# Kernel optimization log

Measured on AMD Instinct MI355X. Metric: run time of the kernel, lower is better.

## Reference

```python
import jax, jax.numpy as jnp
import numpy as np

N = 100000      # nodes
E = 1600000     # edges (before self loops)
F_IN = 128      # input features
HID = 64        # hidden_layer (heads=1)
G = 128         # number of graphs
NUM_CLASSES = 10


def _gat_layer(x, src, dst, W, a_src, a_dst, b):
    # x: [N, Fin] -> h: [N, HID]; single head, PyG GATConv defaults
    h = x @ W
    alpha_src = h @ a_src            # [N]
    alpha_dst = h @ a_dst            # [N]
    e = jax.nn.leaky_relu(alpha_src[src] + alpha_dst[dst], 0.2)   # [E+N]
    # segment softmax over incoming edges of each destination node
    m = jax.ops.segment_max(e, dst, num_segments=N)
    ex = jnp.exp(e - m[dst])
    denom = jax.ops.segment_sum(ex, dst, num_segments=N)
    alpha = ex / denom[dst]
    out = jax.ops.segment_sum(h[src] * alpha[:, None], dst, num_segments=N)
    return out + b


def setup_inputs() -> dict:
    key = jax.random.key(0)
    ks = jax.random.split(key, 16)
    x = jax.random.normal(ks[0], (N, F_IN), dtype=jnp.float32)
    edge_index = jax.random.randint(ks[1], (2, E), 0, N, dtype=jnp.int64)
    edge_weight = jax.random.uniform(ks[2], (E,), dtype=jnp.float32)
    batch = jnp.sort(jax.random.randint(ks[3], (N,), 0, G, dtype=jnp.int64))
    s = 0.1
    params = {
        'W1': jax.random.normal(ks[4], (F_IN, HID), jnp.float32) * s,
        'a_src1': jax.random.normal(ks[5], (HID,), jnp.float32) * s,
        'a_dst1': jax.random.normal(ks[6], (HID,), jnp.float32) * s,
        'b1': jnp.zeros((HID,), jnp.float32),
        'W2': jax.random.normal(ks[7], (HID, HID), jnp.float32) * s,
        'a_src2': jax.random.normal(ks[8], (HID,), jnp.float32) * s,
        'a_dst2': jax.random.normal(ks[9], (HID,), jnp.float32) * s,
        'b2': jnp.zeros((HID,), jnp.float32),
        'lin_w': jax.random.normal(ks[10], (HID, HID // 2), jnp.float32) * s,
        'lin_b': jnp.zeros((HID // 2,), jnp.float32),
        'cls_w': jax.random.normal(ks[11], (HID // 2, NUM_CLASSES), jnp.float32) * s,
        'cls_b': jnp.zeros((NUM_CLASSES,), jnp.float32),
    }
    return {'x': x, 'edge_index': edge_index, 'edge_weight': edge_weight, 'batch': batch, **params}


def reference(x, edge_index, edge_weight, batch,
              W1, a_src1, a_dst1, b1,
              W2, a_src2, a_dst2, b2,
              lin_w, lin_b, cls_w, cls_b):
    # PyG GATConv add_self_loops=True
    loops = jnp.arange(N, dtype=edge_index.dtype)
    src = jnp.concatenate([edge_index[0], loops])
    dst = jnp.concatenate([edge_index[1], loops])
    # edge_weight unused: GATConv built without edge_dim (lin_edge is None)
    h = _gat_layer(x, src, dst, W1, a_src1, a_dst1, b1)
    h = jax.nn.relu(h)
    h = _gat_layer(h, src, dst, W2, a_src2, a_dst2, b2)
    # global_mean_pool over graphs
    counts = jax.ops.segment_sum(jnp.ones((N,), h.dtype), batch, num_segments=G)
    pooled = jax.ops.segment_sum(h, batch, num_segments=G) / jnp.maximum(counts, 1.0)[:, None]
    z = jax.nn.relu(pooled @ lin_w + lin_b)       # dropout p=0 -> identity
    logits = z @ cls_w + cls_b
    return jax.nn.log_softmax(logits, axis=1)     # SSL=False -> deg_pred=0 omitted
```

## Files before the change

### kernel.cpp

```cpp
#include <hip/hip_runtime.h>
#include <hip/hip_bf16.h>

#define NN 100000
#define NE 1600000
#define NT (NE + NN)
#define FIN 128
#define HID 64
#define NG 128
#define NC 10
#define BSHIFT 8
#define NBUCK ((NN + 255) >> 8)
#define A2_EPB 4096
#define PCH 8

typedef __hip_bfloat16 bf16;

__device__ __forceinline__ float ldx(const void* p, size_t i, int f32flag) {
    return f32flag ? ((const float*)p)[i]
                   : __bfloat162float(((const bf16*)p)[i]);
}
__device__ __forceinline__ float b2f(unsigned short u) {
    return __uint_as_float((unsigned)u << 16);
}

__global__ void probe_kernel(const unsigned int* __restrict__ xw,
                             const int* __restrict__ ei,
                             int* __restrict__ flags) {
    if (threadIdx.x != 0 || blockIdx.x != 0) return;
    int f32 = 0;
    for (int i = 0; i < 64; i++) {
        unsigned int u = xw[i];
        float vl = __uint_as_float((u & 0xffffu) << 16);
        float vh = __uint_as_float(u & 0xffff0000u);
        if (!(fabsf(vl) < 1e10f)) f32 = 1;
        if (!(fabsf(vh) < 1e10f)) f32 = 1;
    }
    int i64 = 1;
    for (int i = 0; i < 64; i++)
        if (ei[2 * i + 1] != 0) i64 = 0;
    flags[0] = f32;
    flags[1] = i64;
}

__global__ __launch_bounds__(256) void cparams_kernel(
        const void* p0, const void* p1, const void* p2, const void* p3,
        const void* p4, const void* p5, const void* p6, const void* p7,
        const void* p8, const void* p9, const void* p10, const void* p11,
        const int* __restrict__ flags, float* __restrict__ Pf) {
    const void* ps[12] = {p0,p1,p2,p3,p4,p5,p6,p7,p8,p9,p10,p11};
    const int   sz[12] = {8192,64,64,64,4096,64,64,64,2048,32,320,10};
    const int f = flags[0];
    int off = 0;
    for (int t = 0; t < 12; t++) {
        for (int i = threadIdx.x; i < sz[t]; i += 256)
            Pf[off + i] = ldx(ps[t], i, f);
        off += sz[t];
    }
}

template <int K>
__global__ __launch_bounds__(256) void gemm_kernel(const void* __restrict__ X,
                                                   const float* __restrict__ Wf,
                                                   const float* __restrict__ va,
                                                   const float* __restrict__ vb,
                                                   unsigned char* __restrict__ H8,
                                                   float* __restrict__ AS,
                                                   float* __restrict__ AD,
                                                   const int* __restrict__ flags,
                                                   int force_f32) {
    constexpr int KC = 32;
    constexpr int XLD = KC + 4;
    __shared__ float Wl[KC * HID];
    __shared__ float Xl[64 * XLD];
    const int t = threadIdx.x;
    const int f = force_f32 ? 1 : flags[0];
    const int brow = blockIdx.x * 64;
    const int rt = (t >> 4) * 4;
    const int ct = (t & 15) * 4;
    float acc[4][4] = {};
    for (int kc = 0; kc < K; kc += KC) {
        for (int i = t; i < KC * HID / 4; i += 256)
            ((float4*)Wl)[i] = ((const float4*)(Wf + kc * HID))[i];
        for (int i = t; i < 64 * KC / 4; i += 256) {
            int rr = i >> 3, col = (i & 7) * 4;
            int grow = brow + rr; if (grow >= NN) grow = NN - 1;
            size_t gbase = (size_t)grow * K + kc + col;
            float4 o;
            if (f) {
                o = *(const float4*)((const float*)X + gbase);
            } else {
                ushort4 v = *(const ushort4*)((const bf16*)X + gbase);
                o.x = b2f(v.x); o.y = b2f(v.y); o.z = b2f(v.z); o.w = b2f(v.w);
            }
            *(float4*)&Xl[rr * XLD + col] = o;
        }
        __syncthreads();
        const float* xp = &Xl[rt * XLD];
        const float* wp = &Wl[ct];
#pragma unroll 2
        for (int k = 0; k < KC; k += 4) {
            float4 w0 = *(const float4*)(wp + (k + 0) * HID);
            float4 w1 = *(const float4*)(wp + (k + 1) * HID);
            float4 w2 = *(const float4*)(wp + (k + 2) * HID);
            float4 w3 = *(const float4*)(wp + (k + 3) * HID);
#pragma unroll
            for (int i = 0; i < 4; i++) {
                float4 xv = *(const float4*)(xp + i * XLD + k);
                acc[i][0] += xv.x * w0.x + xv.y * w1.x + xv.z * w2.x + xv.w * w3.x;
                acc[i][1] += xv.x * w0.y + xv.y * w1.y + xv.z * w2.y + xv.w * w3.y;
                acc[i][2] += xv.x * w0.z + xv.y * w1.z + xv.z * w2.z + xv.w * w3.z;
                acc[i][3] += xv.x * w0.w + xv.y * w1.w + xv.z * w2.w + xv.w * w3.w;
            }
        }
        __syncthreads();
    }
    float va4[4], vb4[4];
#pragma unroll
    for (int j = 0; j < 4; j++) { va4[j] = va[ct + j]; vb4[j] = vb[ct + j]; }
#pragma unroll
    for (int i = 0; i < 4; i++) {
        int row = brow + rt + i;
        unsigned pk = 0;
#pragma unroll
        for (int j = 0; j < 4; j++) {
            int q = (int)rintf(fminf(fmaxf(acc[i][j] * 16.f, -128.f), 127.f)) + 128;
            pk |= ((unsigned)q & 0xffu) << (8 * j);
        }
        if (row < NN)
            *(unsigned*)&H8[(size_t)row * HID + ct] = pk;
        float s1 = acc[i][0] * va4[0] + acc[i][1] * va4[1] + acc[i][2] * va4[2] + acc[i][3] * va4[3];
        float s2 = acc[i][0] * vb4[0] + acc[i][1] * vb4[1] + acc[i][2] * vb4[2] + acc[i][3] * vb4[3];
#pragma unroll
        for (int off = 8; off; off >>= 1) {
            s1 += __shfl_xor(s1, off);
            s2 += __shfl_xor(s2, off);
        }
        if ((t & 15) == 0 && row < NN) { AS[row] = s1; AD[row] = s2; }
    }
}

__global__ __launch_bounds__(256) void bhistA_kernel(const int* __restrict__ ei,
                                                     const int* __restrict__ flags,
                                                     int* __restrict__ gcnt) {
    __shared__ int lc[NBUCK];
    for (int i = threadIdx.x; i < NBUCK; i += 256) lc[i] = 0;
    __syncthreads();
    const int i64 = flags[1];
    const int base = blockIdx.x * 8192;
    for (int i = threadIdx.x; i < 8192; i += 256) {
        int e = base + i;
        if (e >= NT) break;
        int d;
        if (e < NE) { long idx = (long)NE + e; d = i64 ? ei[2 * idx] : ei[idx]; }
        else d = e - NE;
        if ((unsigned)d >= NN) d = 0;
        atomicAdd(&lc[d >> BSHIFT], 1);
    }
    __syncthreads();
    for (int i = threadIdx.x; i < NBUCK; i += 256)
        if (lc[i]) atomicAdd(&gcnt[i], lc[i]);
}

__global__ __launch_bounds__(64) void bscan_kernel(const int* __restrict__ gcnt,
                                                   int* __restrict__ gbase,
                                                   int* __restrict__ gcursor) {
    const int lane = threadIdx.x;
    int carry = 0;
    for (int base = 0; base < NBUCK; base += 64) {
        int idx = base + lane;
        int v = (idx < NBUCK) ? gcnt[idx] : 0;
        int x = v;
#pragma unroll
        for (int off = 1; off < 64; off <<= 1) {
            int y = __shfl_up(x, off);
            if (lane >= off) x += y;
        }
        int excl = carry + x - v;
        if (idx < NBUCK) { gbase[idx] = excl; gcursor[idx] = excl; }
        carry += __shfl(x, 63);
    }
    if (lane == 0) gbase[NBUCK] = carry;
}

__global__ __launch_bounds__(256) void bscat_kernel(const int* __restrict__ ei,
                                                    const int* __restrict__ flags,
                                                    int* __restrict__ gcursor,
                                                    int2* __restrict__ bucketA) {
    __shared__ int lc[NBUCK];
    __shared__ int lpos[NBUCK];
    __shared__ int lcur[NBUCK];
    for (int i = threadIdx.x; i < NBUCK; i += 256) { lc[i] = 0; lcur[i] = 0; }
    __syncthreads();
    const int i64 = flags[1];
    const int base = blockIdx.x * A2_EPB;
    int sarr[16], darr[16];
#pragma unroll
    for (int i = 0; i < 16; i++) {
        int e = base + i * 256 + threadIdx.x;
        int s = -1, d = 0;
        if (e < NT) {
            if (e < NE) {
                s = i64 ? ei[2 * (long)e] : ei[e];
                long idx = (long)NE + e;
                d = i64 ? ei[2 * idx] : ei[idx];
            } else s = d = e - NE;
            if ((unsigned)d >= NN) d = 0;
            if ((unsigned)s >= NN) s = 0;
            atomicAdd(&lc[d >> BSHIFT], 1);
        }
        sarr[i] = s; darr[i] = d;
    }
    __syncthreads();
    for (int i = threadIdx.x; i < NBUCK; i += 256)
        lpos[i] = lc[i] ? atomicAdd(&gcursor[i], lc[i]) : 0;
    __syncthreads();
#pragma unroll
    for (int i = 0; i < 16; i++) {
        if (sarr[i] >= 0) {
            int b = darr[i] >> BSHIFT;
            int off = atomicAdd(&lcur[b], 1);
            bucketA[lpos[b] + off] = make_int2(sarr[i], darr[i]);
        }
    }
}

__global__ __launch_bounds__(256) void csr_kernel(const int2* __restrict__ bucketA,
                                                  const int* __restrict__ gbase,
                                                  int* __restrict__ rowptr,
                                                  int* __restrict__ slot) {
    const int b = blockIdx.x;
    const int nbase = b << BSHIFT;
    const int nb = min(256, NN - nbase);
    const int ebeg = gbase[b], eend = gbase[b + 1];
    __shared__ int cnt[256];
    __shared__ int excl[257];
    __shared__ int cur[256];
    const int t = threadIdx.x;
    cnt[t] = 0; cur[t] = 0;
    __syncthreads();
    for (int i = ebeg + t; i < eend; i += 256)
        atomicAdd(&cnt[bucketA[i].y - nbase], 1);
    __syncthreads();
    if (t < 64) {
        int carry = 0;
        for (int s0 = 0; s0 < 256; s0 += 64) {
            int v = cnt[s0 + t];
            int x = v;
#pragma unroll
            for (int off = 1; off < 64; off <<= 1) {
                int y = __shfl_up(x, off);
                if (t >= off) x += y;
            }
            excl[s0 + t] = carry + x - v;
            carry += __shfl(x, 63);
        }
        if (t == 0) excl[256] = carry;
    }
    __syncthreads();
    if (t < nb) rowptr[nbase + t] = ebeg + excl[t];
    if (b == NBUCK - 1 && t == 0) rowptr[NN] = ebeg + excl[nb];
    for (int i = ebeg + t; i < eend; i += 256) {
        int2 ed = bucketA[i];
        int dl = ed.y - nbase;
        int pos = atomicAdd(&cur[dl], 1);
        slot[ebeg + excl[dl] + pos] = ed.x;
    }
}

__global__ __launch_bounds__(256) void edge_kernel(const unsigned char* __restrict__ H8,
                                                   const float* __restrict__ AS,
                                                   const float* __restrict__ AD,
                                                   const int* __restrict__ rowptr,
                                                   const int* __restrict__ slot,
                                                   const float* __restrict__ bias,
                                                   float* __restrict__ OUT,
                                                   int relu_flag) {
    int wid = (blockIdx.x * 256 + threadIdx.x) >> 6;
    int lane = threadIdx.x & 63;
    if (wid >= NN) return;
    const int beg = rowptr[wid], end = rowptr[wid + 1];
    const float ad = AD[wid];
    const int sub = lane >> 4;
    const int fq  = (lane & 15) * 4;
    float a0 = 0.f, a1 = 0.f, a2 = 0.f, a3 = 0.f, dsum = 0.f;
    for (int cbeg = beg; cbeg < end; cbeg += 64) {
        int j = cbeg + lane;
        float ex = 0.f; int s = 0;
        if (j < end) {
            s = slot[j];
            float e = AS[s] + ad;
            e = e > 0.f ? e : 0.2f * e;
            ex = __expf(e);
            dsum += ex;
        }
        int cn = min(64, end - cbeg);
        for (int u = 0; u < cn; u += 8) {
            int   s0 = __shfl(s,  u + sub);
            float e0 = __shfl(ex, u + sub);
            int   s1 = __shfl(s,  u + 4 + sub);
            float e1 = __shfl(ex, u + 4 + sub);
            unsigned w0 = *(const unsigned*)(H8 + (size_t)s0 * HID + fq);
            unsigned w1 = *(const unsigned*)(H8 + (size_t)s1 * HID + fq);
            a0 += e0 * (float)( w0        & 0xffu);
            a1 += e0 * (float)((w0 >>  8) & 0xffu);
            a2 += e0 * (float)((w0 >> 16) & 0xffu);
            a3 += e0 * (float)( w0 >> 24        );
            a0 += e1 * (float)( w1        & 0xffu);
            a1 += e1 * (float)((w1 >>  8) & 0xffu);
            a2 += e1 * (float)((w1 >> 16) & 0xffu);
            a3 += e1 * (float)( w1 >> 24        );
        }
    }
    a0 += __shfl_xor(a0, 16); a0 += __shfl_xor(a0, 32);
    a1 += __shfl_xor(a1, 16); a1 += __shfl_xor(a1, 32);
    a2 += __shfl_xor(a2, 16); a2 += __shfl_xor(a2, 32);
    a3 += __shfl_xor(a3, 16); a3 += __shfl_xor(a3, 32);
#pragma unroll
    for (int off = 32; off; off >>= 1) dsum += __shfl_xor(dsum, off);
    if (lane < 16) {
        float inv = 0.0625f / dsum;
        float4 o;
        o.x = a0 * inv - 8.f + bias[fq + 0];
        o.y = a1 * inv - 8.f + bias[fq + 1];
        o.z = a2 * inv - 8.f + bias[fq + 2];
        o.w = a3 * inv - 8.f + bias[fq + 3];
        if (relu_flag) {
            o.x = fmaxf(o.x, 0.f); o.y = fmaxf(o.y, 0.f);
            o.z = fmaxf(o.z, 0.f); o.w = fmaxf(o.w, 0.f);
        }
        *(float4*)&OUT[(size_t)wid * HID + fq] = o;
    }
}

__global__ __launch_bounds__(256) void pool2a_kernel(const float* __restrict__ O,
                                                     const int* __restrict__ bat,
                                                     const int* __restrict__ flags,
                                                     float* __restrict__ part) {
    const int g = blockIdx.x / PCH;
    const int c = blockIdx.x % PCH;
    const int t = threadIdx.x;
    __shared__ int bnds[2];
    if (t < 2) {
        const int i64 = flags[1];
        int target = g + t;
        int lo = 0, hi = NN;
        while (lo < hi) {
            int mid = (lo + hi) >> 1;
            int v = i64 ? bat[2 * (long)mid] : bat[mid];
            if (v < target) lo = mid + 1; else hi = mid;
        }
        bnds[t] = lo;
    }
    __syncthreads();
    const int gbeg = bnds[0], gend = bnds[1];
    const int len = gend - gbeg;
    const int beg = gbeg + (int)((long)len * c / PCH);
    const int end = gbeg + (int)((long)len * (c + 1) / PCH);
    const int lane = t & 63;
    const int wv = t >> 6;
    float acc = 0.f;
    for (int i = beg + wv; i < end; i += 4)
        acc += O[(size_t)i * HID + lane];
    __shared__ float red[4][64];
    red[wv][lane] = acc;
    __syncthreads();
    if (wv == 0)
        part[(size_t)(g * PCH + c) * HID + lane] =
            red[0][lane] + red[1][lane] + red[2][lane] + red[3][lane];
}

__global__ __launch_bounds__(64) void pool2b_kernel(const float* __restrict__ part,
                                                    const int* __restrict__ bat,
                                                    const int* __restrict__ flags,
                                                    float* __restrict__ pooled) {
    const int g = blockIdx.x;
    const int t = threadIdx.x;
    __shared__ int bnds[2];
    if (t < 2) {
        const int i64 = flags[1];
        int target = g + t;
        int lo = 0, hi = NN;
        while (lo < hi) {
            int mid = (lo + hi) >> 1;
            int v = i64 ? bat[2 * (long)mid] : bat[mid];
            if (v < target) lo = mid + 1; else hi = mid;
        }
        bnds[t] = lo;
    }
    __syncthreads();
    float s = 0.f;
#pragma unroll
    for (int c = 0; c < PCH; c++)
        s += part[(size_t)(g * PCH + c) * HID + t];
    float cntg = (float)(bnds[1] - bnds[0]);
    pooled[g * HID + t] = s / fmaxf(cntg, 1.f);
}

__global__ __launch_bounds__(64) void head_kernel(const float* __restrict__ pooled,
                                                  const float* __restrict__ lw, const float* __restrict__ lb,
                                                  const float* __restrict__ cw, const float* __restrict__ cb,
                                                  float* __restrict__ out) {
    const int g = blockIdx.x;
    const int t = threadIdx.x;
    __shared__ float p[HID];
    __shared__ float z[32];
    __shared__ float lg[NC];
    p[t] = pooled[g * HID + t];
    __syncthreads();
    if (t < 32) {
        float acc = lb[t];
#pragma unroll
        for (int k = 0; k < HID; k++) acc += p[k] * lw[k * 32 + t];
        z[t] = fmaxf(acc, 0.f);
    }
    __syncthreads();
    if (t < NC) {
        float acc = cb[t];
#pragma unroll
        for (int j = 0; j < 32; j++) acc += z[j] * cw[j * NC + t];
        lg[t] = acc;
    }
    __syncthreads();
    if (t < NC) {
        float mx = -1e30f;
#pragma unroll
        for (int c = 0; c < NC; c++) mx = fmaxf(mx, lg[c]);
        float s = 0.f;
#pragma unroll
        for (int c = 0; c < NC; c++) s += __expf(lg[c] - mx);
        out[g * NC + t] = lg[t] - mx - __logf(s);
    }
}

extern "C" void kernel_launch(void* const* d_in, const int* in_sizes, int n_in,
                              void* d_out, int out_size, void* d_ws, size_t ws_size,
                              hipStream_t stream) {
    const void* x   = d_in[0];
    const int*  ei  = (const int*)d_in[1];
    const int*  bat = (const int*)d_in[3];

    char* w = (char*)d_ws;
    int2* bucketA = (int2*)w;  w += sizeof(int2) * NT;
    unsigned char* H8 = (unsigned char*)w; w += sizeof(char) * NN * HID;
    float* O      = (float*)w; w += sizeof(float) * NN * HID;
    float* AS     = (float*)w; w += sizeof(float) * NN;
    float* AD     = (float*)w; w += sizeof(float) * NN;
    int* rowptr   = (int*)w;   w += sizeof(int) * (NN + 1);
    int* slot     = (int*)w;   w += sizeof(int) * NT;
    float* part   = (float*)w; w += sizeof(float) * NG * PCH * HID;
    float* pooled = (float*)w; w += sizeof(float) * NG * HID;
    int* gcnt     = (int*)w;   w += sizeof(int) * NBUCK;
    int* gbase    = (int*)w;   w += sizeof(int) * (NBUCK + 1);
    int* gcursor  = (int*)w;   w += sizeof(int) * NBUCK;
    int* flags    = (int*)w;   w += sizeof(int) * 2;
    float* Pf     = (float*)w; w += sizeof(float) * 16384;

    float* W1f = Pf;             float* as1 = Pf + 8192;
    float* ad1 = Pf + 8256;      float* b1  = Pf + 8320;
    float* W2f = Pf + 8384;      float* as2 = Pf + 12480;
    float* ad2 = Pf + 12544;     float* b2  = Pf + 12608;
    float* lw  = Pf + 12672;     float* lb  = Pf + 14720;
    float* cw  = Pf + 14752;     float* cb  = Pf + 15072;

    hipMemsetAsync(gcnt, 0, sizeof(int) * NBUCK, stream);

    probe_kernel<<<1, 64, 0, stream>>>((const unsigned int*)x, ei, flags);
    cparams_kernel<<<1, 256, 0, stream>>>(d_in[4], d_in[5], d_in[6], d_in[7],
                                          d_in[8], d_in[9], d_in[10], d_in[11],
                                          d_in[12], d_in[13], d_in[14], d_in[15],
                                          flags, Pf);
    bhistA_kernel<<<(NT + 8191) / 8192, 256, 0, stream>>>(ei, flags, gcnt);
    bscan_kernel<<<1, 64, 0, stream>>>(gcnt, gbase, gcursor);
    bscat_kernel<<<(NT + A2_EPB - 1) / A2_EPB, 256, 0, stream>>>(ei, flags, gcursor, bucketA);
    csr_kernel<<<NBUCK, 256, 0, stream>>>(bucketA, gbase, rowptr, slot);
    gemm_kernel<FIN><<<(NN + 63) / 64, 256, 0, stream>>>(x, W1f, as1, ad1, H8, AS, AD, flags, 0);
    edge_kernel<<<NN / 4, 256, 0, stream>>>(H8, AS, AD, rowptr, slot, b1, O, 1);
    gemm_kernel<HID><<<(NN + 63) / 64, 256, 0, stream>>>(O, W2f, as2, ad2, H8, AS, AD, flags, 1);
    edge_kernel<<<NN / 4, 256, 0, stream>>>(H8, AS, AD, rowptr, slot, b2, O, 0);
    pool2a_kernel<<<NG * PCH, 256, 0, stream>>>(O, bat, flags, part);
    pool2b_kernel<<<NG, 64, 0, stream>>>(part, bat, flags, pooled);
    head_kernel<<<NG, 64, 0, stream>>>(pooled, lw, lb, cw, cb, (float*)d_out);
}
```

Baseline: 265.6 us.

## Merge setup kernels, pack edge buckets into int, store hidden as bf16

Three separate ideas are applied. The probe, param conversion and gcnt memset are merged into one setup kernel, and pool2b is merged with the head into a tail kernel, which cuts launch count. Bucketed edges are packed into a single int holding the 17-bit source and 8-bit local destination instead of an int2, halving scatter and CSR traffic. The layer outputs are now stored as bf16 instead of fp32, halving reads and writes for gemm2 and pooling at the cost of extra rounding error in hidden activations.

```diff
diff --git a/kernel.cpp b/kernel.cpp
--- a/kernel.cpp
+++ b/kernel.cpp
@@ -22,34 +22,37 @@
 __device__ __forceinline__ float b2f(unsigned short u) {
     return __uint_as_float((unsigned)u << 16);
 }
-
-__global__ void probe_kernel(const unsigned int* __restrict__ xw,
-                             const int* __restrict__ ei,
-                             int* __restrict__ flags) {
-    if (threadIdx.x != 0 || blockIdx.x != 0) return;
-    int f32 = 0;
-    for (int i = 0; i < 64; i++) {
-        unsigned int u = xw[i];
-        float vl = __uint_as_float((u & 0xffffu) << 16);
-        float vh = __uint_as_float(u & 0xffff0000u);
-        if (!(fabsf(vl) < 1e10f)) f32 = 1;
-        if (!(fabsf(vh) < 1e10f)) f32 = 1;
-    }
-    int i64 = 1;
-    for (int i = 0; i < 64; i++)
-        if (ei[2 * i + 1] != 0) i64 = 0;
-    flags[0] = f32;
-    flags[1] = i64;
-}
-
-__global__ __launch_bounds__(256) void cparams_kernel(
+__device__ __forceinline__ unsigned short f2b(float v) {
+    return (unsigned short)(__float_as_uint(v) >> 16);
+}
+
+__global__ __launch_bounds__(256) void setup_kernel(
+        const unsigned int* __restrict__ xw, const int* __restrict__ ei,
         const void* p0, const void* p1, const void* p2, const void* p3,
         const void* p4, const void* p5, const void* p6, const void* p7,
         const void* p8, const void* p9, const void* p10, const void* p11,
-        const int* __restrict__ flags, float* __restrict__ Pf) {
+        int* __restrict__ flags, int* __restrict__ gcnt, float* __restrict__ Pf) {
+    __shared__ int sf[2];
+    if (threadIdx.x == 0) {
+        int f32 = 0;
+        for (int i = 0; i < 64; i++) {
+            unsigned int u = xw[i];
+            float vl = __uint_as_float((u & 0xffffu) << 16);
+            float vh = __uint_as_float(u & 0xffff0000u);
+            if (!(fabsf(vl) < 1e10f)) f32 = 1;
+            if (!(fabsf(vh) < 1e10f)) f32 = 1;
+        }
+        int i64 = 1;
+        for (int i = 0; i < 64; i++)
+            if (ei[2 * i + 1] != 0) i64 = 0;
+        sf[0] = f32; sf[1] = i64;
+        flags[0] = f32; flags[1] = i64;
+    }
+    for (int i = threadIdx.x; i < NBUCK; i += 256) gcnt[i] = 0;
+    __syncthreads();
+    const int f = sf[0];
     const void* ps[12] = {p0,p1,p2,p3,p4,p5,p6,p7,p8,p9,p10,p11};
     const int   sz[12] = {8192,64,64,64,4096,64,64,64,2048,32,320,10};
-    const int f = flags[0];
     int off = 0;
     for (int t = 0; t < 12; t++) {
         for (int i = threadIdx.x; i < sz[t]; i += 256)
@@ -67,13 +70,13 @@
                                                    float* __restrict__ AS,
                                                    float* __restrict__ AD,
                                                    const int* __restrict__ flags,
-                                                   int force_f32) {
+                                                   int dtype_mode) {
     constexpr int KC = 32;
     constexpr int XLD = KC + 4;
     __shared__ float Wl[KC * HID];
     __shared__ float Xl[64 * XLD];
     const int t = threadIdx.x;
-    const int f = force_f32 ? 1 : flags[0];
+    const int f = (dtype_mode < 0) ? flags[0] : dtype_mode;
     const int brow = blockIdx.x * 64;
     const int rt = (t >> 4) * 4;
     const int ct = (t & 15) * 4;
@@ -185,7 +188,7 @@
 __global__ __launch_bounds__(256) void bscat_kernel(const int* __restrict__ ei,
                                                     const int* __restrict__ flags,
                                                     int* __restrict__ gcursor,
-                                                    int2* __restrict__ bucketA) {
+                                                    int* __restrict__ bucketA) {
     __shared__ int lc[NBUCK];
     __shared__ int lpos[NBUCK];
     __shared__ int lcur[NBUCK];
@@ -219,12 +222,12 @@
         if (sarr[i] >= 0) {
             int b = darr[i] >> BSHIFT;
             int off = atomicAdd(&lcur[b], 1);
-            bucketA[lpos[b] + off] = make_int2(sarr[i], darr[i]);
-        }
-    }
-}
-
-__global__ __launch_bounds__(256) void csr_kernel(const int2* __restrict__ bucketA,
+            bucketA[lpos[b] + off] = ((darr[i] & 0xff) << 17) | sarr[i];
+        }
+    }
+}
+
+__global__ __launch_bounds__(256) void csr_kernel(const int* __restrict__ bucketA,
                                                   const int* __restrict__ gbase,
                                                   int* __restrict__ rowptr,
                                                   int* __restrict__ slot) {
@@ -239,7 +242,7 @@
     cnt[t] = 0; cur[t] = 0;
     __syncthreads();
     for (int i = ebeg + t; i < eend; i += 256)
-        atomicAdd(&cnt[bucketA[i].y - nbase], 1);
+        atomicAdd(&cnt[bucketA[i] >> 17], 1);
     __syncthreads();
     if (t < 64) {
         int carry = 0;
@@ -260,10 +263,10 @@
     if (t < nb) rowptr[nbase + t] = ebeg + excl[t];
     if (b == NBUCK - 1 && t == 0) rowptr[NN] = ebeg + excl[nb];
     for (int i = ebeg + t; i < eend; i += 256) {
-        int2 ed = bucketA[i];
-        int dl = ed.y - nbase;
+        int v = bucketA[i];
+        int dl = v >> 17;
         int pos = atomicAdd(&cur[dl], 1);
-        slot[ebeg + excl[dl] + pos] = ed.x;
+        slot[ebeg + excl[dl] + pos] = v & 0x1ffff;
     }
 }
 
@@ -273,7 +276,7 @@
                                                    const int* __restrict__ rowptr,
                                                    const int* __restrict__ slot,
                                                    const float* __restrict__ bias,
-                                                   float* __restrict__ OUT,
+                                                   bf16* __restrict__ OUT,
                                                    int relu_flag) {
     int wid = (blockIdx.x * 256 + threadIdx.x) >> 6;
     int lane = threadIdx.x & 63;
@@ -319,20 +322,21 @@
     for (int off = 32; off; off >>= 1) dsum += __shfl_xor(dsum, off);
     if (lane < 16) {
         float inv = 0.0625f / dsum;
-        float4 o;
-        o.x = a0 * inv - 8.f + bias[fq + 0];
-        o.y = a1 * inv - 8.f + bias[fq + 1];
-        o.z = a2 * inv - 8.f + bias[fq + 2];
-        o.w = a3 * inv - 8.f + bias[fq + 3];
+        float ox = a0 * inv - 8.f + bias[fq + 0];
+        float oy = a1 * inv - 8.f + bias[fq + 1];
+        float oz = a2 * inv - 8.f + bias[fq + 2];
+        float ow = a3 * inv - 8.f + bias[fq + 3];
         if (relu_flag) {
-            o.x = fmaxf(o.x, 0.f); o.y = fmaxf(o.y, 0.f);
-            o.z = fmaxf(o.z, 0.f); o.w = fmaxf(o.w, 0.f);
-        }
-        *(float4*)&OUT[(size_t)wid * HID + fq] = o;
-    }
-}
-
-__global__ __launch_bounds__(256) void pool2a_kernel(const float* __restrict__ O,
+            ox = fmaxf(ox, 0.f); oy = fmaxf(oy, 0.f);
+            oz = fmaxf(oz, 0.f); ow = fmaxf(ow, 0.f);
+        }
+        ushort4 pk;
+        pk.x = f2b(ox); pk.y = f2b(oy); pk.z = f2b(oz); pk.w = f2b(ow);
+        *(ushort4*)&OUT[(size_t)wid * HID + fq] = pk;
+    }
+}
+
+__global__ __launch_bounds__(256) void pool2a_kernel(const bf16* __restrict__ O,
                                                      const int* __restrict__ bat,
                                                      const int* __restrict__ flags,
                                                      float* __restrict__ part) {
@@ -360,7 +364,7 @@
     const int wv = t >> 6;
     float acc = 0.f;
     for (int i = beg + wv; i < end; i += 4)
-        acc += O[(size_t)i * HID + lane];
+        acc += __bfloat162float(O[(size_t)i * HID + lane]);
     __shared__ float red[4][64];
     red[wv][lane] = acc;
     __syncthreads();
@@ -369,13 +373,18 @@
             red[0][lane] + red[1][lane] + red[2][lane] + red[3][lane];
 }
 
-__global__ __launch_bounds__(64) void pool2b_kernel(const float* __restrict__ part,
-                                                    const int* __restrict__ bat,
-                                                    const int* __restrict__ flags,
-                                                    float* __restrict__ pooled) {
+__global__ __launch_bounds__(64) void tail_kernel(const float* __restrict__ part,
+                                                  const int* __restrict__ bat,
+                                                  const int* __restrict__ flags,
+                                                  const float* __restrict__ lw, const float* __restrict__ lb,
+                                                  const float* __restrict__ cw, const float* __restrict__ cb,
+                                                  float* __restrict__ out) {
     const int g = blockIdx.x;
     const int t = threadIdx.x;
     __shared__ int bnds[2];
+    __shared__ float p[HID];
+    __shared__ float z[32];
+    __shared__ float lg[NC];
     if (t < 2) {
         const int i64 = flags[1];
         int target = g + t;
@@ -388,24 +397,12 @@
         bnds[t] = lo;
     }
     __syncthreads();
-    float s = 0.f;
+    float s0 = 0.f;
 #pragma unroll
     for (int c = 0; c < PCH; c++)
-        s += part[(size_t)(g * PCH + c) * HID + t];
+        s0 += part[(size_t)(g * PCH + c) * HID + t];
     float cntg = (float)(bnds[1] - bnds[0]);
-    pooled[g * HID + t] = s / fmaxf(cntg, 1.f);
-}
-
-__global__ __launch_bounds__(64) void head_kernel(const float* __restrict__ pooled,
-                                                  const float* __restrict__ lw, const float* __restrict__ lb,
-                                                  const float* __restrict__ cw, const float* __restrict__ cb,
-                                                  float* __restrict__ out) {
-    const int g = blockIdx.x;
-    const int t = threadIdx.x;
-    __shared__ float p[HID];
-    __shared__ float z[32];
-    __shared__ float lg[NC];
-    p[t] = pooled[g * HID + t];
+    p[t] = s0 / fmaxf(cntg, 1.f);
     __syncthreads();
     if (t < 32) {
         float acc = lb[t];
@@ -440,15 +437,14 @@
     const int*  bat = (const int*)d_in[3];
 
     char* w = (char*)d_ws;
-    int2* bucketA = (int2*)w;  w += sizeof(int2) * NT;
+    int* bucketA  = (int*)w;   w += sizeof(int) * NT;
     unsigned char* H8 = (unsigned char*)w; w += sizeof(char) * NN * HID;
-    float* O      = (float*)w; w += sizeof(float) * NN * HID;
+    bf16* Obf     = (bf16*)w;  w += sizeof(bf16) * NN * HID;
     float* AS     = (float*)w; w += sizeof(float) * NN;
     float* AD     = (float*)w; w += sizeof(float) * NN;
     int* rowptr   = (int*)w;   w += sizeof(int) * (NN + 1);
     int* slot     = (int*)w;   w += sizeof(int) * NT;
     float* part   = (float*)w; w += sizeof(float) * NG * PCH * HID;
-    float* pooled = (float*)w; w += sizeof(float) * NG * HID;
     int* gcnt     = (int*)w;   w += sizeof(int) * NBUCK;
     int* gbase    = (int*)w;   w += sizeof(int) * (NBUCK + 1);
     int* gcursor  = (int*)w;   w += sizeof(int) * NBUCK;
@@ -462,22 +458,19 @@
     float* lw  = Pf + 12672;     float* lb  = Pf + 14720;
     float* cw  = Pf + 14752;     float* cb  = Pf + 15072;
 
-    hipMemsetAsync(gcnt, 0, sizeof(int) * NBUCK, stream);
-
-    probe_kernel<<<1, 64, 0, stream>>>((const unsigned int*)x, ei, flags);
-    cparams_kernel<<<1, 256, 0, stream>>>(d_in[4], d_in[5], d_in[6], d_in[7],
-                                          d_in[8], d_in[9], d_in[10], d_in[11],
-                                          d_in[12], d_in[13], d_in[14], d_in[15],
-                                          flags, Pf);
+    setup_kernel<<<1, 256, 0, stream>>>((const unsigned int*)x, ei,
+                                        d_in[4], d_in[5], d_in[6], d_in[7],
+                                        d_in[8], d_in[9], d_in[10], d_in[11],
+                                        d_in[12], d_in[13], d_in[14], d_in[15],
+                                        flags, gcnt, Pf);
     bhistA_kernel<<<(NT + 8191) / 8192, 256, 0, stream>>>(ei, flags, gcnt);
     bscan_kernel<<<1, 64, 0, stream>>>(gcnt, gbase, gcursor);
     bscat_kernel<<<(NT + A2_EPB - 1) / A2_EPB, 256, 0, stream>>>(ei, flags, gcursor, bucketA);
     csr_kernel<<<NBUCK, 256, 0, stream>>>(bucketA, gbase, rowptr, slot);
-    gemm_kernel<FIN><<<(NN + 63) / 64, 256, 0, stream>>>(x, W1f, as1, ad1, H8, AS, AD, flags, 0);
-    edge_kernel<<<NN / 4, 256, 0, stream>>>(H8, AS, AD, rowptr, slot, b1, O, 1);
-    gemm_kernel<HID><<<(NN + 63) / 64, 256, 0, stream>>>(O, W2f, as2, ad2, H8, AS, AD, flags, 1);
-    edge_kernel<<<NN / 4, 256, 0, stream>>>(H8, AS, AD, rowptr, slot, b2, O, 0);
-    pool2a_kernel<<<NG * PCH, 256, 0, stream>>>(O, bat, flags, part);
-    pool2b_kernel<<<NG, 64, 0, stream>>>(part, bat, flags, pooled);
-    head_kernel<<<NG, 64, 0, stream>>>(pooled, lw, lb, cw, cb, (float*)d_out);
-}
+    gemm_kernel<FIN><<<(NN + 63) / 64, 256, 0, stream>>>(x, W1f, as1, ad1, H8, AS, AD, flags, -1);
+    edge_kernel<<<NN / 4, 256, 0, stream>>>(H8, AS, AD, rowptr, slot, b1, Obf, 1);
+    gemm_kernel<HID><<<(NN + 63) / 64, 256, 0, stream>>>(Obf, W2f, as2, ad2, H8, AS, AD, flags, 0);
+    edge_kernel<<<NN / 4, 256, 0, stream>>>(H8, AS, AD, rowptr, slot, b2, Obf, 0);
+    pool2a_kernel<<<NG * PCH, 256, 0, stream>>>(Obf, bat, flags, part);
+    tail_kernel<<<NG, 64, 0, stream>>>(part, bat, flags, lw, lb, cw, cb, (float*)d_out);
+}
```

Measured after the change: 257.1 us. -3.2%, faster.
